# Performance work log

Hardware: AMD Instinct MI355X
Metric: run time of the kernel (lower is better)

The kernel has to match this reference:

```python
import jax, jax.numpy as jnp
import numpy as np

H = 16  # n_heads
D = 64  # d_keys


def setup_inputs() -> dict:
    key = jax.random.key(0)
    ks = jax.random.split(key, 11)
    b, n, dm = 2, 2048, 1024
    s = 1.0 / np.sqrt(dm)
    return {
        "q": jax.random.normal(ks[0], (b, n, dm), jnp.float32),
        "k": jax.random.normal(ks[1], (b, n, dm), jnp.float32),
        "v": jax.random.normal(ks[2], (b, n, dm), jnp.float32),
        "Wq": jax.random.normal(ks[3], (dm, H * D), jnp.float32) * s,
        "bq": jax.random.normal(ks[4], (H * D,), jnp.float32) * 0.01,
        "Wk": jax.random.normal(ks[5], (dm, H * D), jnp.float32) * s,
        "bk": jax.random.normal(ks[6], (H * D,), jnp.float32) * 0.01,
        "Wv": jax.random.normal(ks[7], (dm, H * D), jnp.float32) * s,
        "bv": jax.random.normal(ks[8], (H * D,), jnp.float32) * 0.01,
        "Wo": jax.random.normal(ks[9], (H * D, dm), jnp.float32) * s,
        "bo": jax.random.normal(ks[10], (dm,), jnp.float32) * 0.01,
    }


def reference(q, k, v, Wq, bq, Wk, bk, Wv, bv, Wo, bo):
    b, n_q, _ = q.shape
    n_k = k.shape[1]
    # projections -> [b, n, h, d]
    qh = (q @ Wq + bq).reshape(b, n_q, H, D)
    kh = (k @ Wk + bk).reshape(b, n_k, H, D)
    vh = (v @ Wv + bv).reshape(b, n_k, H, D)
    # scores [b, h, n, m]
    scores = jnp.einsum('bnhd,bmhd->bhnm', qh, kh)
    causal = jnp.triu(jnp.ones((n_q, n_k), dtype=bool), k=1)  # True above diag
    scores = jnp.where(causal, -jnp.inf, scores)
    att = jax.nn.softmax(scores / np.sqrt(D).astype(np.float32), axis=-1)
    att_out = jnp.einsum('bhnm,bmhd->bnhd', att, vh).reshape(b, n_q, H * D)
    return att_out @ Wo + bo
```

## Files before the change

kernel.cpp:

```cpp
#include <hip/hip_runtime.h>

typedef float f32x4 __attribute__((ext_vector_type(4)));
typedef __bf16 bf16x8 __attribute__((ext_vector_type(8)));
typedef __bf16 bf16x4 __attribute__((ext_vector_type(4)));
typedef __bf16 bf16_t;

#define NH 16
#define DH 64
#define SEQ 2048
#define DM 1024

#define QSCALE 0.18033688f

extern "C" hipError_t hipMemPtrGetInfo(void* ptr, size_t* size);

__device__ __forceinline__ bf16x8 ld8(const bf16_t* p) { return *(const bf16x8*)p; }
__device__ __forceinline__ void st8(bf16_t* p, bf16x8 v) { *(bf16x8*)p = v; }

__device__ __forceinline__ void gl_lds16(const bf16_t* g, bf16_t* l)
{
    __builtin_amdgcn_global_load_lds(
        (const __attribute__((address_space(1))) unsigned int*)g,
        (__attribute__((address_space(3))) unsigned int*)l, 16, 0, 0);
}

__global__ __launch_bounds__(256) void fill_sentinel(float* out, unsigned n, float val)
{
    unsigned stride = gridDim.x * blockDim.x;
    for (unsigned i = blockIdx.x * blockDim.x + threadIdx.x; i < n; i += stride)
        out[i] = val;
}

__global__ __launch_bounds__(256) void prep(
    const float* __restrict__ q, const float* __restrict__ k,
    const float* __restrict__ v,
    const float* __restrict__ w0, const float* __restrict__ w1,
    const float* __restrict__ w2, const float* __restrict__ w3,
    bf16_t* __restrict__ xb, bf16_t* __restrict__ wt, int fragmode)
{
    int z = blockIdx.z;
    if (z < 3) {
        const float* src = (z == 0) ? q : (z == 1) ? k : v;
        bf16_t* dst = xb + (size_t)z * (4096u * 1024u);
        size_t i8 = ((size_t)blockIdx.x * 256 + threadIdx.x) * 8;
        f32x4 u = *(const f32x4*)(src + i8);
        f32x4 w = *(const f32x4*)(src + i8 + 4);
        bf16x8 h = { (bf16_t)u.x, (bf16_t)u.y, (bf16_t)u.z, (bf16_t)u.w,
                     (bf16_t)w.x, (bf16_t)w.y, (bf16_t)w.z, (bf16_t)w.w };
        st8(dst + i8, h);
    } else {
        int x = blockIdx.x;
        if (x >= 1024) return;
        int w = x >> 8, rem = x & 255;
        int bx = rem & 15, by = rem >> 4;
        const float* in = (w == 0) ? w0 : (w == 1) ? w1 : (w == 2) ? w2 : w3;
        bf16_t* out = wt + (size_t)w * DM * DM;
        __shared__ __align__(16) bf16_t tile[64][72];
        int t = threadIdx.x;
        int k0 = by * 64, n0 = bx * 64;
        int r0 = t >> 4, c0 = (t & 15) * 4;
        for (int p = 0; p < 4; p++) {
            int r = r0 + p * 16;
            const float* src = in + (size_t)(k0 + r) * DM + n0 + c0;
            for (int i = 0; i < 4; i++) tile[r][c0 + i] = (bf16_t)src[i];
        }
        __syncthreads();
        if (fragmode && w < 3) {
            int idx = t;
            #pragma unroll
            for (int p = 0; p < 2; p++, idx += 256) {
                int rn = idx & 63;
                int kc8 = idx >> 6;
                int n_abs = n0 + rn;
                int rblk = n_abs >> 4, l16v = n_abs & 15;
                int kk = kc8 >> 2, gg = kc8 & 3;
                bf16x8 vv;
                for (int j = 0; j < 8; j++) vv[j] = tile[kc8 * 8 + j][rn];
                st8(out + (size_t)((rblk * 16 + by) * 2 + kk) * 512
                        + (gg * 16 + l16v) * 8, vv);
            }
        } else {
            for (int p = 0; p < 4; p++) {
                int rn = r0 + p * 16;
                bf16_t* dst = out + (size_t)(n0 + rn) * DM + k0 + c0;
                for (int i = 0; i < 4; i++) dst[i] = tile[c0 + i][rn];
            }
        }
    }
}

#define LGKM0 asm volatile("s_waitcnt lgkmcnt(0)" ::: "memory")
#define VMC(n) asm volatile("s_waitcnt vmcnt(" #n ")" ::: "memory")
#define BARRIER __builtin_amdgcn_s_barrier()

#define STA(d, h, dk) do { \
    _Pragma("unroll") for (int j = 0; j < 2; j++) \
        gl_lds16(Xp + ((h) * 128 + j * 64) * DM + (dk) * 64, \
                 Ab + sdst0 + ((d) * 2 + (h)) * 8192 + j * 4096); } while (0)
#define RDA(d, h, F) do { \
    _Pragma("unroll") for (int mf = 0; mf < 4; mf++) { \
        F[mf][0] = ld8(Ab + rA0 + ((d) * 2 + (h)) * 8192 + mf * 1024); \
        F[mf][1] = ld8(Ab + rA1 + ((d) * 2 + (h)) * 8192 + mf * 1024); } } while (0)
#define LDB(SET, nh, kto) do { \
    _Pragma("unroll") for (int nf = 0; nf < 2; nf++) \
        _Pragma("unroll") for (int kk = 0; kk < 2; kk++) \
            SET[nf][kk] = ld8(Bp + (nh) * 131072 + nf * 16384 \
                              + (kto) * 1024 + kk * 512); } while (0)
#define MMQ(AF, BF, Q) do { \
    __builtin_amdgcn_s_setprio(1); \
    _Pragma("unroll") for (int mf = 0; mf < 4; mf++) \
        _Pragma("unroll") for (int nf = 0; nf < 2; nf++) { \
            Q[mf][nf] = __builtin_amdgcn_mfma_f32_16x16x32_bf16( \
                AF[mf][0], BF[nf][0], Q[mf][nf], 0, 0, 0); \
            Q[mf][nf] = __builtin_amdgcn_mfma_f32_16x16x32_bf16( \
                AF[mf][1], BF[nf][1], Q[mf][nf], 0, 0, 0); } \
    __builtin_amdgcn_s_setprio(0); } while (0)

__global__ __launch_bounds__(512, 2) void gemm8(
    const bf16_t* __restrict__ xall, const bf16_t* __restrict__ bfall,
    const float* __restrict__ b0v, const float* __restrict__ b1v,
    const float* __restrict__ b2v, bf16_t* __restrict__ outall)
{
    int z = blockIdx.z;
    int mode = z;
    const bf16_t* X  = xall  + (size_t)z * (4096u * 1024u);
    const bf16_t* Bf = bfall + (size_t)z * (1024u * 1024u);
    const float* bias = (z == 0) ? b0v : (z == 1) ? b1v : b2v;
    bf16_t* out = outall + (size_t)z * (4096u * 1024u);

    int m0 = blockIdx.x * 256;
    int n0 = blockIdx.y * 256;

    __shared__ __align__(16) bf16_t Ab[2 * 2 * 128 * 64];

    int tid  = threadIdx.x;
    int lane = tid & 63, w = tid >> 6;
    int g = lane >> 4, l16 = lane & 15;
    int wm = w >> 2, wn = w & 3;
    int rl = lane >> 3, cl = lane & 7;
    int w8 = w * 8;

    int srow = w8 + rl;
    int scol = (cl ^ rl) * 8;
    const bf16_t* Xp = X + (size_t)(m0 + srow) * DM + scol;
    int sdst0 = w8 * 64 + lane * 8;

    int x7 = l16 & 7;
    int rA0 = (wm * 64 + l16) * 64 + ((0 + g) ^ x7) * 8;
    int rA1 = (wm * 64 + l16) * 64 + ((4 + g) ^ x7) * 8;

    const bf16_t* Bp = Bf + ((size_t)(n0 >> 4) + wn * 2) * 16384 + lane * 8;

    f32x4 a00[4][2] = {}, a01[4][2] = {}, a10[4][2] = {}, a11[4][2] = {};
    bf16x8 afA[4][2], afB[4][2], Ba[2][2], Bb[2][2];

    STA(0, 0, 0); STA(0, 1, 0); STA(1, 0, 1); STA(1, 1, 1);
    LDB(Ba, 0, 0); LDB(Bb, 1, 0);
    VMC(0);
    BARRIER;
    RDA(0, 0, afA);

    #pragma unroll 1
    for (int i = 0; i < 7; i++) {
        VMC(6); LGKM0; MMQ(afA, Ba, a00); BARRIER;
        STA(0, 0, 2); VMC(4); RDA(0, 1, afB); MMQ(afA, Bb, a01); BARRIER;
        LGKM0; MMQ(afB, Ba, a10); LDB(Ba, 0, 1); BARRIER;
        MMQ(afB, Bb, a11); LDB(Bb, 1, 1); STA(0, 1, 2); RDA(1, 0, afA); BARRIER;
        VMC(6); LGKM0; MMQ(afA, Ba, a00); BARRIER;
        STA(1, 0, 3); VMC(4); RDA(1, 1, afB); MMQ(afA, Bb, a01); BARRIER;
        LGKM0; MMQ(afB, Ba, a10); LDB(Ba, 0, 2); BARRIER;
        MMQ(afB, Bb, a11); LDB(Bb, 1, 2); STA(1, 1, 3); RDA(0, 0, afA); BARRIER;
        Xp += 128; Bp += 2048;
    }
    VMC(6); LGKM0; MMQ(afA, Ba, a00); BARRIER;
    VMC(2); RDA(0, 1, afB); MMQ(afA, Bb, a01); BARRIER;
    LGKM0; MMQ(afB, Ba, a10); LDB(Ba, 0, 1); BARRIER;
    MMQ(afB, Bb, a11); LDB(Bb, 1, 1); RDA(1, 0, afA); BARRIER;
    VMC(4); LGKM0; MMQ(afA, Ba, a00); BARRIER;
    VMC(0); RDA(1, 1, afB); MMQ(afA, Bb, a01); BARRIER;
    LGKM0; MMQ(afB, Ba, a10); BARRIER;
    MMQ(afB, Bb, a11);

    float scale = (mode == 0) ? QSCALE : 1.0f;
#define EPI(Q, Mh, Nh) do { \
    _Pragma("unroll") for (int mf = 0; mf < 4; mf++) { \
        int mbase = m0 + (Mh) * 128 + wm * 64 + mf * 16 + g * 4; \
        int bb = mbase >> 11, nn0 = mbase & 2047; \
        _Pragma("unroll") for (int nf = 0; nf < 2; nf++) { \
            int col = n0 + (Nh) * 128 + wn * 32 + nf * 16 + l16; \
            float bv = bias[col]; \
            int hh = col >> 6, dd = col & 63; \
            if (mode == 2) { \
                bf16x4 pv; \
                for (int r = 0; r < 4; r++) pv[r] = (bf16_t)(Q[mf][nf][r] + bv); \
                *(bf16x4*)(out + ((size_t)(bb * NH + hh) * DH + dd) * SEQ + nn0) = pv; \
            } else { \
                for (int r = 0; r < 4; r++) \
                    out[((size_t)(bb * NH + hh) * SEQ + nn0 + r) * DH + dd] = \
                        (bf16_t)((Q[mf][nf][r] + bv) * scale); \
            } } } } while (0)
    EPI(a00, 0, 0); EPI(a01, 0, 1); EPI(a10, 1, 0); EPI(a11, 1, 1);
#undef EPI
}

__global__ __launch_bounds__(256) void gemm_out(
    const bf16_t* __restrict__ X, const bf16_t* __restrict__ WT,
    const float* __restrict__ bias, bf16_t* __restrict__ out,
    float* __restrict__ outf, int out_is_f32)
{
    int m0 = blockIdx.x * 128;
    int n0 = blockIdx.y * 128;

    __shared__ __align__(16) bf16_t Alds[128 * 64];
    __shared__ __align__(16) bf16_t Blds[128 * 64];

    int t = threadIdx.x;
    int lane = t & 63, wave = t >> 6;
    int g = lane >> 4, l16 = lane & 15;
    int wr0 = (wave >> 1) * 64, wc0 = (wave & 1) * 64;
    int crow = lane >> 3;
    int ccol = (lane & 7) * 8;

    f32x4 acc[4][4] = {};

    for (int k0 = 0; k0 < DM; k0 += 64) {
        __syncthreads();
        for (int c = wave; c < 16; c += 4) {
            int row = c * 8 + crow;
            gl_lds16(X  + (size_t)(m0 + row) * DM + k0 + ccol,
                     Alds + c * 512 + lane * 8);
            gl_lds16(WT + (size_t)(n0 + row) * DM + k0 + ccol,
                     Blds + c * 512 + lane * 8);
        }
        __syncthreads();
        for (int kk = 0; kk < 2; kk++) {
            bf16x8 af[4], bfr[4];
            for (int i = 0; i < 4; i++)
                af[i] = ld8(Alds + (wr0 + i * 16 + l16) * 64 + kk * 32 + g * 8);
            for (int i = 0; i < 4; i++)
                bfr[i] = ld8(Blds + (wc0 + i * 16 + l16) * 64 + kk * 32 + g * 8);
            for (int mi = 0; mi < 4; mi++)
                for (int ni = 0; ni < 4; ni++)
                    acc[mi][ni] = __builtin_amdgcn_mfma_f32_16x16x32_bf16(
                        af[mi], bfr[ni], acc[mi][ni], 0, 0, 0);
        }
    }
    for (int mi = 0; mi < 4; mi++) {
        int mbase = m0 + wr0 + mi * 16 + g * 4;
        for (int ni = 0; ni < 4; ni++) {
            int col = n0 + wc0 + ni * 16 + l16;
            float bv = bias[col];
            for (int r = 0; r < 4; r++) {
                float sv = acc[mi][ni][r] + bv;
                if (out_is_f32) outf[(size_t)(mbase + r) * 1024 + col] = sv;
                else            out[(size_t)(mbase + r) * 1024 + col] = (bf16_t)sv;
            }
        }
    }
}

__global__ __launch_bounds__(256) void gemm_mha(
    const float* __restrict__ x0, const float* __restrict__ x1,
    const float* __restrict__ x2, const bf16_t* __restrict__ xb,
    const bf16_t* __restrict__ wt_base,
    const float* __restrict__ b0, const float* __restrict__ b1,
    const float* __restrict__ b2, bf16_t* __restrict__ out_base,
    float* __restrict__ outf, int mode_base, int out_is_f32)
{
    int z = blockIdx.z;
    const float* Xf    = (z == 0) ? x0 : (z == 1) ? x1 : x2;
    const bf16_t* WT   = wt_base + (size_t)z * DM * DM;
    const float* bias  = (z == 0) ? b0 : (z == 1) ? b1 : b2;
    bf16_t* out = out_base + (size_t)z * (4096u * 1024u);
    int mode = mode_base + z;

    int m0 = blockIdx.x * 128;
    int n0 = blockIdx.y * 128;

    __shared__ __align__(16) bf16_t Alds[128 * 64];
    __shared__ __align__(16) bf16_t Blds[128 * 64];

    int t = threadIdx.x;
    int lane = t & 63, wave = t >> 6;
    int g = lane >> 4, l16 = lane & 15;
    int wr0 = (wave >> 1) * 64, wc0 = (wave & 1) * 64;

    f32x4 acc[4][4] = {};
    int srow = t >> 3, sk = (t & 7) * 8;

    for (int k0 = 0; k0 < DM; k0 += 64) {
        __syncthreads();
        if (mode < 3) {
            for (int p = 0; p < 4; p++) {
                int r = srow + p * 32;
                const float* s4 = Xf + (size_t)(m0 + r) * DM + k0 + sk;
                f32x4 u = *(const f32x4*)s4;
                f32x4 w = *(const f32x4*)(s4 + 4);
                bf16x8 h = { (bf16_t)u.x, (bf16_t)u.y, (bf16_t)u.z, (bf16_t)u.w,
                             (bf16_t)w.x, (bf16_t)w.y, (bf16_t)w.z, (bf16_t)w.w };
                st8(Alds + r * 64 + sk, h);
            }
        } else {
            for (int p = 0; p < 4; p++) {
                int r = srow + p * 32;
                st8(Alds + r * 64 + sk, ld8(xb + (size_t)(m0 + r) * DM + k0 + sk));
            }
        }
        for (int p = 0; p < 4; p++) {
            int r = srow + p * 32;
            st8(Blds + r * 64 + sk, ld8(WT + (size_t)(n0 + r) * DM + k0 + sk));
        }
        __syncthreads();
        for (int kk = 0; kk < 2; kk++) {
            bf16x8 af[4], bfr[4];
            for (int i = 0; i < 4; i++)
                af[i] = ld8(Alds + (wr0 + i * 16 + l16) * 64 + kk * 32 + g * 8);
            for (int i = 0; i < 4; i++)
                bfr[i] = ld8(Blds + (wc0 + i * 16 + l16) * 64 + kk * 32 + g * 8);
            for (int mi = 0; mi < 4; mi++)
                for (int ni = 0; ni < 4; ni++)
                    acc[mi][ni] = __builtin_amdgcn_mfma_f32_16x16x32_bf16(
                        af[mi], bfr[ni], acc[mi][ni], 0, 0, 0);
        }
    }
    float scale = (mode == 0) ? QSCALE : 1.0f;
    for (int mi = 0; mi < 4; mi++) {
        int mbase = m0 + wr0 + mi * 16 + g * 4;
        for (int ni = 0; ni < 4; ni++) {
            int col = n0 + wc0 + ni * 16 + l16;
            float bv = bias[col];
            if (mode == 2) {
                int bb = mbase >> 11, nn0 = mbase & 2047;
                int h = col >> 6, d = col & 63;
                bf16x4 pv;
                for (int r = 0; r < 4; r++) pv[r] = (bf16_t)(acc[mi][ni][r] + bv);
                *(bf16x4*)(out + ((size_t)(bb * NH + h) * DH + d) * SEQ + nn0) = pv;
            } else {
                for (int r = 0; r < 4; r++) {
                    int mr = mbase + r;
                    float sv = (acc[mi][ni][r] + bv) * scale;
                    if (mode == 3) {
                        if (out_is_f32) outf[(size_t)mr * 1024 + col] = sv;
                        else            out[(size_t)mr * 1024 + col] = (bf16_t)sv;
                    } else {
                        int bb = mr >> 11, nn = mr & 2047;
                        int h = col >> 6, d = col & 63;
                        out[((size_t)(bb * NH + h) * SEQ + nn) * DH + d] = (bf16_t)sv;
                    }
                }
            }
        }
    }
}

__global__ __launch_bounds__(512) void attn(
    const bf16_t* __restrict__ Qh, const bf16_t* __restrict__ Kh,
    const bf16_t* __restrict__ VT, bf16_t* __restrict__ att)
{
    int bhx = blockIdx.x;
    int yy  = blockIdx.y;
    int p   = (yy < 8) ? yy : 23 - yy;
    int TB  = 2 * p + 2;

    const bf16_t* Qb = Qh + (size_t)bhx * SEQ * DH;
    const bf16_t* Kb = Kh + (size_t)bhx * SEQ * DH;
    const bf16_t* Vb = VT + (size_t)bhx * DH * SEQ;

    __shared__ __align__(16) bf16_t Klds[2][64 * 72];
    __shared__ __align__(16) bf16_t Vlds[2][64 * 72];
    __shared__ __align__(16) bf16_t Plds[8][16 * 72];

    int t = threadIdx.x, lane = t & 63, wave = t >> 6;
    int g = lane >> 4, l16 = lane & 15;
    int srow = t >> 3, sk = (t & 7) * 8;
    int qt = 2 * p + (wave >> 2);
    int Tw = qt + 1;
    int rowl = (wave & 3) * 16 + l16;

    bf16x8 qf[2];
    for (int kk = 0; kk < 2; kk++)
        qf[kk] = ld8(Qb + (size_t)(qt * 64 + rowl) * DH + kk * 32 + g * 8);

    f32x4 accO[4] = {};
    float l = 0.f;
    bf16_t* Pw = Plds[wave];

    st8(&Klds[0][srow * 72 + sk], ld8(Kb + (size_t)srow * DH + sk));
    st8(&Vlds[0][srow * 72 + sk], ld8(Vb + (size_t)srow * SEQ + sk));

    for (int j = 0; j < TB; j++) {
        __syncthreads();
        bool pre = (j + 1 < TB);
        bf16x8 kreg, vreg;
        if (pre) {
            kreg = ld8(Kb + (size_t)((j + 1) * 64 + srow) * DH + sk);
            vreg = ld8(Vb + (size_t)srow * SEQ + (j + 1) * 64 + sk);
        }
        if (j < Tw) {
            int buf = j & 1;
            bool diag = (j == Tw - 1);

            f32x4 s[4];
            __builtin_amdgcn_s_setprio(1);
            for (int c = 0; c < 4; c++) {
                f32x4 a = {};
                for (int kk = 0; kk < 2; kk++) {
                    bf16x8 kf = ld8(&Klds[buf][(c * 16 + l16) * 72 + kk * 32 + g * 8]);
                    a = __builtin_amdgcn_mfma_f32_16x16x32_bf16(kf, qf[kk], a, 0, 0, 0);
                }
                s[c] = a;
            }
            __builtin_amdgcn_s_setprio(0);
            for (int c = 0; c < 4; c++) {
                bf16x4 pv;
                for (int r = 0; r < 4; r++) {
                    float v = s[c][r];
                    if (diag && (c * 16 + g * 4 + r) > rowl) v = -1e30f;
                    float pe;
                    asm("v_exp_f32 %0, %1" : "=v"(pe) : "v"(v));
                    l += pe;
                    pv[r] = (bf16_t)pe;
                }
                *(bf16x4*)(Pw + l16 * 72 + c * 16 + g * 4) = pv;
            }
            asm volatile("s_waitcnt lgkmcnt(0)" ::: "memory");

            bf16x8 pf0 = ld8(Pw + l16 * 72 + g * 8);
            bf16x8 pf1 = ld8(Pw + l16 * 72 + 32 + g * 8);
            __builtin_amdgcn_s_setprio(1);
            for (int c2 = 0; c2 < 4; c2++) {
                bf16x8 vf0 = ld8(&Vlds[buf][(c2 * 16 + l16) * 72 + g * 8]);
                accO[c2] = __builtin_amdgcn_mfma_f32_16x16x32_bf16(vf0, pf0, accO[c2], 0, 0, 0);
                bf16x8 vf1 = ld8(&Vlds[buf][(c2 * 16 + l16) * 72 + 32 + g * 8]);
                accO[c2] = __builtin_amdgcn_mfma_f32_16x16x32_bf16(vf1, pf1, accO[c2], 0, 0, 0);
            }
            __builtin_amdgcn_s_setprio(0);

            if (diag) {
                float lt = l;
                lt += __shfl_xor(lt, 16);
                lt += __shfl_xor(lt, 32);
                float inv = 1.f / lt;
                int qabs = qt * 64 + rowl;
                int bb = bhx >> 4, h = bhx & 15;
                for (int c2 = 0; c2 < 4; c2++) {
                    bf16x4 ov;
                    for (int r = 0; r < 4; r++) ov[r] = (bf16_t)(accO[c2][r] * inv);
                    *(bf16x4*)(att + (((size_t)bb * SEQ + qabs) * NH + h) * DH
                               + c2 * 16 + g * 4) = ov;
                }
            }
        }
        if (pre) {
            int b = (j + 1) & 1;
            st8(&Klds[b][srow * 72 + sk], kreg);
            st8(&Vlds[b][srow * 72 + sk], vreg);
        }
    }
}

extern "C" void kernel_launch(void* const* d_in, const int* in_sizes, int n_in,
                              void* d_out, int out_size, void* d_ws, size_t ws_size,
                              hipStream_t stream) {
    const float* q  = (const float*)d_in[0];
    const float* k  = (const float*)d_in[1];
    const float* v  = (const float*)d_in[2];
    const float* Wq = (const float*)d_in[3];
    const float* bq = (const float*)d_in[4];
    const float* Wk = (const float*)d_in[5];
    const float* bk = (const float*)d_in[6];
    const float* Wv = (const float*)d_in[7];
    const float* bv = (const float*)d_in[8];
    const float* Wo = (const float*)d_in[9];
    const float* bo = (const float*)d_in[10];

    const size_t MAT = 1024u * 1024u;
    const size_t BIG = 4096u * 1024u;
    const size_t NEED_BASE = 64 + (4 * BIG + 4 * MAT) * 2;
    const size_t NEED_FAST = NEED_BASE + 3 * BIG * 2;

    if (ws_size < NEED_BASE) {
        fill_sentinel<<<1024, 256, 0, stream>>>((float*)d_out,
                                                (unsigned)out_size, 100.0f);
        return;
    }

    int out_is_f32 = 1;
    size_t osz = 0;
    if (hipMemPtrGetInfo(d_out, &osz) == hipSuccess && osz != 0 &&
        osz < (size_t)out_size * 4)
        out_is_f32 = 0;

    bf16_t* base = (bf16_t*)d_ws + 32;
    bf16_t* Qh  = base;
    bf16_t* Kh  = Qh + BIG;
    bf16_t* VT  = Kh + BIG;
    bf16_t* att = VT + BIG;
    bf16_t* WT  = att + BIG;
    bf16_t* Xb  = WT + 4 * MAT;

    if (ws_size >= NEED_FAST) {
        prep<<<dim3(2048, 1, 4), 256, 0, stream>>>(q, k, v, Wq, Wk, Wv, Wo,
                                                   Xb, WT, 1);
        gemm8<<<dim3(16, 4, 3), 512, 0, stream>>>(Xb, WT, bq, bk, bv, Qh);
        attn<<<dim3(32, 16), 512, 0, stream>>>(Qh, Kh, VT, att);
        gemm_out<<<dim3(32, 8), 256, 0, stream>>>(att, WT + 3 * MAT, bo,
                                                  (bf16_t*)d_out, (float*)d_out,
                                                  out_is_f32);
    } else {
        prep<<<dim3(2048, 1, 4), 256, 0, stream>>>(q, k, v, Wq, Wk, Wv, Wo,
                                                   (bf16_t*)d_ws, WT, 0);
        gemm_mha<<<dim3(32, 8, 3), 256, 0, stream>>>(q, k, v, nullptr, WT,
                                                     bq, bk, bv, Qh, nullptr, 0, 0);
        attn<<<dim3(32, 16), 512, 0, stream>>>(Qh, Kh, VT, att);
        gemm_mha<<<dim3(32, 8, 1), 256, 0, stream>>>(nullptr, nullptr, nullptr, att,
                                                     WT + 3 * MAT, bo, bo, bo,
                                                     (bf16_t*)d_out, (float*)d_out,
                                                     3, out_is_f32);
    }
}
```

Baseline: 225.2 us.

## Split long causal attention rows across two blocks and combine partials

```diff
diff --git a/kernel.cpp b/kernel.cpp
--- a/kernel.cpp
+++ b/kernel.cpp
@@ -353,6 +353,162 @@
     }
 }
 
+__constant__ unsigned char JP[24] = {7,15,15,14,14,6,13,13,12,12,5,11,
+                                     11,10,10,4,9,9,8,8,3,2,1,0};
+__constant__ unsigned char JS[24] = {0,0,1,0,1,0,0,1,0,1,0,0,
+                                     1,0,1,0,0,1,0,1,0,0,0,0};
+
+__global__ __launch_bounds__(512) void attn_split(
+    const bf16_t* __restrict__ Qh, const bf16_t* __restrict__ Kh,
+    const bf16_t* __restrict__ VT, bf16_t* __restrict__ att,
+    float* __restrict__ Pb, float* __restrict__ Lb)
+{
+    int bhx = blockIdx.x;
+    int y   = blockIdx.y;
+    int p   = JP[y];
+    int seg = JS[y];
+    bool splitf = (p >= 8);
+    int k0 = splitf ? seg * (p + 1) : 0;
+    int k1 = splitf ? k0 + (p + 1) : 2 * p + 2;
+
+    const bf16_t* Qb = Qh + (size_t)bhx * SEQ * DH;
+    const bf16_t* Kb = Kh + (size_t)bhx * SEQ * DH;
+    const bf16_t* Vb = VT + (size_t)bhx * DH * SEQ;
+
+    __shared__ __align__(16) bf16_t Klds[2][64 * 72];
+    __shared__ __align__(16) bf16_t Vlds[2][64 * 72];
+    __shared__ __align__(16) bf16_t Plds[8][16 * 72];
+
+    int t = threadIdx.x, lane = t & 63, wave = t >> 6;
+    int g = lane >> 4, l16 = lane & 15;
+    int srow = t >> 3, sk = (t & 7) * 8;
+    int qt = 2 * p + (wave >> 2);
+    int Tw = qt + 1;
+    int rowl = (wave & 3) * 16 + l16;
+
+    bf16x8 qf[2];
+    for (int kk = 0; kk < 2; kk++)
+        qf[kk] = ld8(Qb + (size_t)(qt * 64 + rowl) * DH + kk * 32 + g * 8);
+
+    f32x4 accO[4] = {};
+    float l = 0.f;
+    bf16_t* Pw = Plds[wave];
+
+    st8(&Klds[0][srow * 72 + sk], ld8(Kb + (size_t)(k0 * 64 + srow) * DH + sk));
+    st8(&Vlds[0][srow * 72 + sk], ld8(Vb + (size_t)srow * SEQ + k0 * 64 + sk));
+
+    for (int j = k0; j < k1; j++) {
+        __syncthreads();
+        bool pre = (j + 1 < k1);
+        bf16x8 kreg, vreg;
+        if (pre) {
+            kreg = ld8(Kb + (size_t)((j + 1) * 64 + srow) * DH + sk);
+            vreg = ld8(Vb + (size_t)srow * SEQ + (j + 1) * 64 + sk);
+        }
+        if (j < Tw) {
+            int buf = (j - k0) & 1;
+            bool diag = (j == Tw - 1);
+
+            f32x4 s[4];
+            __builtin_amdgcn_s_setprio(1);
+            for (int c = 0; c < 4; c++) {
+                f32x4 a = {};
+                for (int kk = 0; kk < 2; kk++) {
+                    bf16x8 kf = ld8(&Klds[buf][(c * 16 + l16) * 72 + kk * 32 + g * 8]);
+                    a = __builtin_amdgcn_mfma_f32_16x16x32_bf16(kf, qf[kk], a, 0, 0, 0);
+                }
+                s[c] = a;
+            }
+            __builtin_amdgcn_s_setprio(0);
+            for (int c = 0; c < 4; c++) {
+                bf16x4 pv;
+                for (int r = 0; r < 4; r++) {
+                    float v = s[c][r];
+                    if (diag && (c * 16 + g * 4 + r) > rowl) v = -1e30f;
+                    float pe;
+                    asm("v_exp_f32 %0, %1" : "=v"(pe) : "v"(v));
+                    l += pe;
+                    pv[r] = (bf16_t)pe;
+                }
+                *(bf16x4*)(Pw + l16 * 72 + c * 16 + g * 4) = pv;
+            }
+            asm volatile("s_waitcnt lgkmcnt(0)" ::: "memory");
+
+            bf16x8 pf0 = ld8(Pw + l16 * 72 + g * 8);
+            bf16x8 pf1 = ld8(Pw + l16 * 72 + 32 + g * 8);
+            __builtin_amdgcn_s_setprio(1);
+            for (int c2 = 0; c2 < 4; c2++) {
+                bf16x8 vf0 = ld8(&Vlds[buf][(c2 * 16 + l16) * 72 + g * 8]);
+                accO[c2] = __builtin_amdgcn_mfma_f32_16x16x32_bf16(vf0, pf0, accO[c2], 0, 0, 0);
+                bf16x8 vf1 = ld8(&Vlds[buf][(c2 * 16 + l16) * 72 + 32 + g * 8]);
+                accO[c2] = __builtin_amdgcn_mfma_f32_16x16x32_bf16(vf1, pf1, accO[c2], 0, 0, 0);
+            }
+            __builtin_amdgcn_s_setprio(0);
+
+            if (diag && !splitf) {
+                float lt = l;
+                lt += __shfl_xor(lt, 16);
+                lt += __shfl_xor(lt, 32);
+                float inv = 1.f / lt;
+                int qabs = qt * 64 + rowl;
+                int bb = bhx >> 4, h = bhx & 15;
+                for (int c2 = 0; c2 < 4; c2++) {
+                    bf16x4 ov;
+                    for (int r = 0; r < 4; r++) ov[r] = (bf16_t)(accO[c2][r] * inv);
+                    *(bf16x4*)(att + (((size_t)bb * SEQ + qabs) * NH + h) * DH
+                               + c2 * 16 + g * 4) = ov;
+                }
+            }
+        }
+        if (pre) {
+            int b = (j - k0 + 1) & 1;
+            st8(&Klds[b][srow * 72 + sk], kreg);
+            st8(&Vlds[b][srow * 72 + sk], vreg);
+        }
+    }
+
+    if (splitf) {
+        float lt = l;
+        lt += __shfl_xor(lt, 16);
+        lt += __shfl_xor(lt, 32);
+        int slot = (bhx * 16 + (qt - 16)) * 2 + seg;
+        float* Pp = Pb + (size_t)slot * 4096 + rowl * 64;
+        #pragma unroll
+        for (int c2 = 0; c2 < 4; c2++)
+            *(f32x4*)(Pp + c2 * 16 + g * 4) = accO[c2];
+        if (g == 0) Lb[slot * 64 + rowl] = lt;
+    }
+}
+
+__global__ __launch_bounds__(256) void attn_combine(
+    const float* __restrict__ Pb, const float* __restrict__ Lb,
+    bf16_t* __restrict__ att)
+{
+    int bhx = blockIdx.x, q16 = blockIdx.y;
+    int qt = 16 + q16;
+    int t = threadIdx.x;
+    int row = t >> 2, dc = (t & 3) * 16;
+
+    int slot0 = (bhx * 16 + q16) * 2;
+    int slot1 = slot0 + 1;
+    float lsum = Lb[slot0 * 64 + row] + Lb[slot1 * 64 + row];
+    float inv = 1.f / lsum;
+
+    const float* P0 = Pb + (size_t)slot0 * 4096 + row * 64 + dc;
+    const float* P1 = Pb + (size_t)slot1 * 4096 + row * 64 + dc;
+    int qabs = qt * 64 + row;
+    int bb = bhx >> 4, h = bhx & 15;
+    bf16_t* ob = att + (((size_t)bb * SEQ + qabs) * NH + h) * DH + dc;
+    #pragma unroll
+    for (int c = 0; c < 4; c++) {
+        f32x4 a = *(const f32x4*)(P0 + c * 4);
+        f32x4 b = *(const f32x4*)(P1 + c * 4);
+        bf16x4 ov;
+        for (int r = 0; r < 4; r++) ov[r] = (bf16_t)((a[r] + b[r]) * inv);
+        *(bf16x4*)(ob + c * 4) = ov;
+    }
+}
+
 __global__ __launch_bounds__(512) void attn(
     const bf16_t* __restrict__ Qh, const bf16_t* __restrict__ Kh,
     const bf16_t* __restrict__ VT, bf16_t* __restrict__ att)
@@ -500,10 +656,13 @@
     bf16_t* Xb  = WT + 4 * MAT;
 
     if (ws_size >= NEED_FAST) {
+        float* Pb = (float*)Xb;
+        float* Lb = Pb + (size_t)1024 * 4096;
         prep<<<dim3(2048, 1, 4), 256, 0, stream>>>(q, k, v, Wq, Wk, Wv, Wo,
                                                    Xb, WT, 1);
         gemm8<<<dim3(16, 4, 3), 512, 0, stream>>>(Xb, WT, bq, bk, bv, Qh);
-        attn<<<dim3(32, 16), 512, 0, stream>>>(Qh, Kh, VT, att);
+        attn_split<<<dim3(32, 24), 512, 0, stream>>>(Qh, Kh, VT, att, Pb, Lb);
+        attn_combine<<<dim3(32, 16), 256, 0, stream>>>(Pb, Lb, att);
         gemm_out<<<dim3(32, 8), 256, 0, stream>>>(att, WT + 3 * MAT, bo,
                                                   (bf16_t*)d_out, (float*)d_out,
                                                   out_is_f32);
```

Result: no change. 227.5 us (+1.0%).
